# Performance work log

Measured on AMD Instinct MI355X. Metric: run time of the kernel, lower is better.

Reference implementation:

```python
import jax, jax.numpy as jnp
import numpy as np


def conv2d(x, w, pad):
    # x: [N,C,H,W], w: [O,I,kh,kw]
    return jax.lax.conv_general_dilated(
        x, w, window_strides=(1, 1), padding=[(pad, pad), (pad, pad)],
        dimension_numbers=("NCHW", "OIHW", "NCHW"))


def group_norm1(x, g, b, eps=1e-5):
    # GroupNorm(1, C): normalize over (C,H,W) per sample, per-channel affine
    mu = jnp.mean(x, axis=(1, 2, 3), keepdims=True)
    var = jnp.mean((x - mu) ** 2, axis=(1, 2, 3), keepdims=True)
    xn = (x - mu) * jax.lax.rsqrt(var + eps)
    return xn * g[None, :, None, None] + b[None, :, None, None]


def maxpool_3x3_s2(x):
    return jax.lax.reduce_window(
        x, -jnp.inf, jax.lax.max, (1, 1, 3, 3), (1, 1, 2, 2),
        ((0, 0), (0, 0), (1, 1), (1, 1)))


def hr2o_layer(x, wq, wk, wv, wo, g, b):
    # x: [N,C,H,W]; pairwise attention over the N ROIs at each (h,w)
    q = conv2d(x, wq, 1)
    k = conv2d(x, wk, 1)
    v = conv2d(x, wv, 1)
    scale = 1.0 / jnp.sqrt(jnp.asarray(x.shape[1], x.dtype))
    # torch: (q.unsqueeze(1) * k.unsqueeze(0)).sum(2) == einsum over channels
    att = jnp.einsum("nchw,mchw->nmhw", q, k) * scale  # [N,N,H,W]
    att = jax.nn.softmax(att, axis=1)                    # softmax over keys (dim=1)
    virt = jnp.einsum("nmhw,mchw->nchw", att, v)        # [N,C,H,W]
    virt = jax.nn.relu(group_norm1(virt, g, b))
    virt = conv2d(virt, wo, 1)
    return x + virt  # dropout is identity in eval mode


def setup_inputs() -> dict:
    key = jax.random.key(0)
    ks = jax.random.split(key, 12)
    N, C_R, H, W, HID, NCLS, DEPTH = 64, 1024, 16, 16, 512, 60, 2
    s = 0.02
    return {
        "bg_feats": jax.random.normal(ks[0], (C_R, H, W), jnp.float32),
        "actor_feats": jax.random.normal(ks[1], (N, C_R), jnp.float32),
        "w_conv1": jax.random.normal(ks[2], (HID, 2 * C_R, 1, 1), jnp.float32) * s,
        "w_conv2": jax.random.normal(ks[3], (HID, HID, 3, 3), jnp.float32) * s,
        "w_q": jax.random.normal(ks[4], (DEPTH, HID, HID, 3, 3), jnp.float32) * s,
        "w_k": jax.random.normal(ks[5], (DEPTH, HID, HID, 3, 3), jnp.float32) * s,
        "w_v": jax.random.normal(ks[6], (DEPTH, HID, HID, 3, 3), jnp.float32) * s,
        "w_o": jax.random.normal(ks[7], (DEPTH, HID, HID, 3, 3), jnp.float32) * s,
        "gamma": jnp.ones((DEPTH, HID), jnp.float32),
        "beta": jnp.zeros((DEPTH, HID), jnp.float32),
        "w_fc1": jax.random.normal(ks[8], (HID, C_R), jnp.float32) * s,
        "w_fc2": jax.random.normal(ks[9], (NCLS, 2 * HID), jnp.float32) * s,
    }


def reference(bg_feats, actor_feats, w_conv1, w_conv2, w_q, w_k, w_v, w_o,
              gamma, beta, w_fc1, w_fc2):
    N = actor_feats.shape[0]
    C_R, H, W = bg_feats.shape
    # bg repeated per ROI, actor features tiled over spatial dims
    bg = jnp.broadcast_to(bg_feats[None], (N, C_R, H, W))
    tiled = jnp.broadcast_to(actor_feats[:, :, None, None], (N, C_R, H, W))
    x = jnp.concatenate([bg, tiled], axis=1)           # [N, 2*C_R, H, W]
    x = jax.nn.relu(conv2d(x, w_conv1, 0))             # 1x1 -> [N,HID,H,W]
    x = jax.nn.relu(conv2d(x, w_conv2, 0))             # 3x3 pad=0 -> H-2,W-2
    x = maxpool_3x3_s2(x)                              # -> 7x7
    for d in range(w_q.shape[0]):
        x = hr2o_layer(x, w_q[d], w_k[d], w_v[d], w_o[d], gamma[d], beta[d])
    high_order = jnp.mean(x, axis=(2, 3))              # gap -> [N,HID]
    roi = jax.nn.relu(actor_feats @ w_fc1.T)           # [N,HID]
    out = jnp.concatenate([roi, high_order], axis=1) @ w_fc2.T  # [N,num_classes]
    return out
```

## Files before the change

### kernel.cpp

```cpp
#include <hip/hip_runtime.h>
#include <math.h>


typedef __bf16 bf16x8 __attribute__((ext_vector_type(8)));
typedef float  f32x4  __attribute__((ext_vector_type(4)));

#define NROI 64
#define CR   1024
#define HIDC 512
#define NCLS 60
#define PLANE (NROI * HIDC * 49)
#define ROWH 40
#define OCALL 4608
#define TAPSTR ((size_t)OCALL * 512)
#define WL (HIDC * HIDC * 9)
#define GNCNT 25088.0f

#if defined(__has_builtin)
#  if __has_builtin(__builtin_amdgcn_global_load_lds)
#    define HAVE_GLL 1
#  endif
#endif

__device__ __forceinline__ void stage16(const void* g, void* lds_base, int lane) {
#ifdef HAVE_GLL
    __builtin_amdgcn_global_load_lds(
        (const __attribute__((address_space(1))) unsigned int*)g,
        (__attribute__((address_space(3))) unsigned int*)lds_base, 16, 0, 0);
#else
    *(uint4*)((char*)lds_base + lane * 16) = *(const uint4*)g;
#endif
}

__device__ __forceinline__ float bf2f(unsigned short h) {
    union { unsigned u; float f; } x; x.u = (unsigned)h << 16; return x.f;
}

__global__ __launch_bounds__(256) void k_misc(
    const float* __restrict__ w2, const float* __restrict__ wq,
    const float* __restrict__ wk, const float* __restrict__ wv,
    const float* __restrict__ wo, const float* __restrict__ bg,
    __bf16* __restrict__ wAll, __bf16* __restrict__ inT7,
    __bf16* __restrict__ bgT)
{
    const int b = blockIdx.x, tid = threadIdx.x;
    if (b < 4608) {
        const int bid = b;
        const float* src;
        if (bid < 512) src = w2 + (size_t)bid * 4608;
        else if (bid < 2048) {
            const int r = bid - 512;
            const float* bb = r < 512 ? wq : (r < 1024 ? wk : wv);
            src = bb + (size_t)(r & 511) * 4608;
        } else if (bid < 2560) src = wo + (size_t)(bid - 2048) * 4608;
        else if (bid < 4096) {
            const int r = bid - 2560;
            const float* bb = r < 512 ? wq : (r < 1024 ? wk : wv);
            src = bb + WL + (size_t)(r & 511) * 4608;
        } else src = wo + WL + (size_t)(bid - 4096) * 4608;
        __shared__ float s[4608];
        const float4* s4 = (const float4*)src;
        for (int i = tid; i < 1152; i += 256) ((float4*)s)[i] = s4[i];
        __syncthreads();
        unsigned* dst = (unsigned*)wAll;
        const int c = tid * 2;
        const int swz = ((c >> 3) & 3) ^ ((bid >> 1) & 3);
        const size_t cidx = (size_t)(c >> 5) * 32 + swz * 8 + (c & 7);
#pragma unroll
        for (int t = 0; t < 9; ++t) {
            const unsigned short u0 = __builtin_bit_cast(unsigned short, (__bf16)s[c * 9 + t]);
            const unsigned short u1 = __builtin_bit_cast(unsigned short, (__bf16)s[(c + 1) * 9 + t]);
            dst[((size_t)t * TAPSTR + (size_t)bid * 512 + cidx) / 2] =
                ((unsigned)u1 << 16) | u0;
        }
    } else if (b < 5120) {
        const int k = b - 4608;
        const int n = k >> 3;
        const int j0 = (k & 7) * 4;
#pragma unroll
        for (int i = 0; i < 4; ++i) {
            const int jj = j0 + i;
            int sp;
            if (jj < 9) sp = jj;
            else if (jj < 18) sp = 63 + jj;
            else { const int t = jj - 18; sp = (1 + (t >> 1)) * 9 + (t & 1) * 8; }
            unsigned* d = (unsigned*)(inT7 + ((size_t)n * 81 + sp) * 512);
            d[tid] = 0u;
        }
    } else {
        const int cb = (b - 5120) * 8;
        const int p = tid;
        bf16x8 v;
#pragma unroll
        for (int j = 0; j < 8; ++j)
            v[j] = (__bf16)bg[(size_t)(cb + j) * 256 + p];
        *(bf16x8*)(bgT + (size_t)p * 1024 + cb) = v;
    }
}

__global__ __launch_bounds__(256, 2) void k_ab(
    const __bf16* __restrict__ bgT, const float* __restrict__ actor,
    const float* __restrict__ w1, const float* __restrict__ wfc1,
    float* __restrict__ A_T, float* __restrict__ Bp, float* __restrict__ roi)
{
    const int bx = blockIdx.x, by = blockIdx.y;
    const bool isA = bx < 4;
    const bool isRoi = (bx == 5);
    const int ocWg = by * 64;
    const int tid = threadIdx.x;
    const int w = tid >> 6, lane = tid & 63;
    const int q = lane >> 4, l16 = lane & 15;

    __shared__ __align__(16) __bf16 s_a[64 * ROWH];
    __shared__ __align__(16) __bf16 s_b[64 * ROWH];

    f32x4 acc[4];
#pragma unroll
    for (int nt = 0; nt < 4; ++nt) acc[nt] = (f32x4){0.f, 0.f, 0.f, 0.f};

    const int row = tid >> 2, part = tid & 3;
    for (int ch = 0; ch < 32; ++ch) {
        const int c0 = ch * 32;
        __syncthreads();
        if (isA) {
            const uint4 vv = *(const uint4*)(
                bgT + (size_t)(bx * 64 + row) * 1024 + c0 + part * 8);
            *(uint4*)(&s_a[row * ROWH + part * 8]) = vv;
        } else {
            const float* src = actor + (size_t)row * CR + c0 + part * 8;
            bf16x8 val;
#pragma unroll
            for (int j = 0; j < 8; ++j) val[j] = (__bf16)src[j];
            *(bf16x8*)(&s_a[row * ROWH + part * 8]) = val;
        }
        {
            const float* srcb = isRoi
                ? (wfc1 + (size_t)(ocWg + row) * CR + c0 + part * 8)
                : (w1 + (size_t)(ocWg + row) * (2 * CR)
                      + (isA ? 0 : CR) + c0 + part * 8);
            bf16x8 vb;
#pragma unroll
            for (int j = 0; j < 8; ++j) vb[j] = (__bf16)srcb[j];
            *(bf16x8*)(&s_b[row * ROWH + part * 8]) = vb;
        }
        __syncthreads();
        const bf16x8 af = *(const bf16x8*)(&s_a[(w * 16 + l16) * ROWH + q * 8]);
#pragma unroll
        for (int nt = 0; nt < 4; ++nt) {
            const bf16x8 bw = *(const bf16x8*)(&s_b[(nt * 16 + l16) * ROWH + q * 8]);
            acc[nt] = __builtin_amdgcn_mfma_f32_16x16x32_bf16(af, bw, acc[nt], 0, 0, 0);
        }
    }
#pragma unroll
    for (int r = 0; r < 4; ++r) {
#pragma unroll
        for (int nt = 0; nt < 4; ++nt) {
            const int mrow = w * 16 + q * 4 + r;
            const int oc = ocWg + nt * 16 + l16;
            if (isA)       A_T[(size_t)(bx * 64 + mrow) * 512 + oc] = acc[nt][r];
            else if (isRoi) roi[(size_t)mrow * 512 + oc] = fmaxf(acc[nt][r], 0.f);
            else           Bp[(size_t)mrow * 512 + oc] = acc[nt][r];
        }
    }
}

__global__ __launch_bounds__(256) void k_prep_in2(
    const float* __restrict__ A_T, const float* __restrict__ B,
    __bf16* __restrict__ dst)
{
    const int vn = blockIdx.x;
    const int n = vn >> 2, quad = vn & 3;
    const int sp0 = blockIdx.y * 27;
    const float b0 = B[n * HIDC + threadIdx.x];
    const float b1 = B[n * HIDC + 256 + threadIdx.x];
    for (int sp = sp0; sp < sp0 + 27; ++sp) {
        const int r = sp / 9, w = sp % 9;
        const int p16 = ((quad >> 1) * 7 + r) * 16 + (quad & 1) * 7 + w;
        __bf16* d = dst + ((size_t)vn * 81 + sp) * 512;
        d[threadIdx.x]       = (__bf16)fmaxf(A_T[p16 * HIDC + threadIdx.x] + b0, 0.f);
        d[256 + threadIdx.x] = (__bf16)fmaxf(A_T[p16 * HIDC + 256 + threadIdx.x] + b1, 0.f);
    }
}

template<int VN, bool GNIN>
__global__ __launch_bounds__(256, 2) void k_conv_mfma(
    const __bf16* __restrict__ inT,
    const float* __restrict__ vin,
    const float* __restrict__ statsRaw,
    const float* __restrict__ gamma, const float* __restrict__ beta,
    const __bf16* __restrict__ wAll, int ocBaseGl,
    const float* __restrict__ resid, float* __restrict__ outf,
    __bf16* __restrict__ outb, __bf16* __restrict__ inT7out,
    float* __restrict__ zeroStats, float* __restrict__ gapOut,
    float* __restrict__ gapZero, int mode)
{
    constexpr int MT = (VN == 4) ? 4 : ((VN == 2) ? 2 : 1);
    const int tid = threadIdx.x;
    const int w = tid >> 6, lane = tid & 63;
    const int q = lane >> 4, l16 = lane & 15;
    const int vn_l = (VN == 4) ? w : ((VN == 2) ? (w & 1) : 0);
    const int mh   = (VN == 4) ? 0 : ((VN == 2) ? (w >> 1) : w);
    const int vnBase = blockIdx.x * VN;
    const int ocWg = blockIdx.y * 64;

    if (zeroStats && blockIdx.x == 0 && blockIdx.y == 0 && tid < 128)
        zeroStats[tid] = 0.f;
    if (gapZero && blockIdx.y == 0 && blockIdx.x < 16) {
        const float4 z = {0.f, 0.f, 0.f, 0.f};
        ((float4*)gapZero)[blockIdx.x * 512 + tid * 2]     = z;
        ((float4*)gapZero)[blockIdx.x * 512 + tid * 2 + 1] = z;
    }

    __shared__ __align__(16) __bf16 s_w[9 * 64 * 32];
    __shared__ __align__(16) __bf16 s_in[VN * 81 * ROWH];
    __shared__ float s_mi[VN][2];
    __shared__ float s_gb[GNIN ? 1024 : 4];

    if (GNIN) {
        for (int k = tid; k < 512; k += 256) {
            s_gb[k]       = gamma[k];
            s_gb[512 + k] = beta[k];
        }
        if (tid < VN) {
            const float S = statsRaw[(vnBase + tid) * 2];
            const float Q = statsRaw[(vnBase + tid) * 2 + 1];
            const float mean = S / GNCNT;
            const float var  = Q / GNCNT - mean * mean;
            s_mi[tid][0] = mean;
            s_mi[tid][1] = rsqrtf(var + 1e-5f);
        }
    }

    const int bSwz = (q ^ ((l16 >> 1) & 3)) << 3;
    int aBase[MT];
#pragma unroll
    for (int mt = 0; mt < MT; ++mt) {
        int p = (mh * MT + mt) * 16 + l16;
        p = p > 48 ? 48 : p;
        aBase[mt] = (vn_l * 81 + (p / 7) * 9 + (p % 7)) * ROWH + q * 8;
    }

    f32x4 acc[MT][4];
#pragma unroll
    for (int a = 0; a < MT; ++a)
#pragma unroll
        for (int b = 0; b < 4; ++b) acc[a][b] = (f32x4){0.f, 0.f, 0.f, 0.f};

    for (int ch = 0; ch < 16; ++ch) {
        const int c0 = ch * 32;
        __syncthreads();
#pragma unroll
        for (int i = 0; i < 9; ++i) {
            const int s0 = (w * 9 + i) * 64;
            const int s = s0 + lane;
            const int t = s >> 8;
            const int rem = s & 255;
            const int row = rem >> 2, part = rem & 3;
            const __bf16* g = wAll + (size_t)t * TAPSTR
                + (size_t)(ocBaseGl + ocWg + row) * 512 + c0 + part * 8;
            stage16(g, (char*)s_w + (size_t)s0 * 16, lane);
        }
        for (int idx = tid; idx < VN * 324; idx += 256) {
            const int vnl = idx / 324, rem = idx - vnl * 324;
            const int r = rem >> 2, part = rem & 3;
            if (GNIN) {
                const int rr = r / 9, cc = r % 9;
                bf16x8 val;
                if (rr >= 1 && rr <= 7 && cc >= 1 && cc <= 7) {
                    const int p = (rr - 1) * 7 + (cc - 1);
                    const float* src = vin +
                        ((size_t)(vnBase + vnl) * 49 + p) * 512 + c0 + part * 8;
                    const float m = s_mi[vnl][0], iv = s_mi[vnl][1];
#pragma unroll
                    for (int j = 0; j < 8; ++j)
                        val[j] = (__bf16)fmaxf(
                            (src[j] - m) * iv * s_gb[c0 + part * 8 + j]
                            + s_gb[512 + c0 + part * 8 + j], 0.f);
                } else {
#pragma unroll
                    for (int j = 0; j < 8; ++j) val[j] = (__bf16)0.f;
                }
                *(bf16x8*)(&s_in[(vnl * 81 + r) * ROWH + part * 8]) = val;
            } else {
                const uint4 vv = *(const uint4*)(
                    inT + ((size_t)(vnBase + vnl) * 81 + r) * 512 + c0 + part * 8);
                *(uint4*)(&s_in[(vnl * 81 + r) * ROWH + part * 8]) = vv;
            }
        }
        __syncthreads();
#pragma unroll
        for (int t = 0; t < 9; ++t) {
            const int tOffA = ((t / 3) * 9 + (t % 3)) * ROWH;
            bf16x8 bw[4];
#pragma unroll
            for (int nt = 0; nt < 4; ++nt)
                bw[nt] = *(const bf16x8*)(&s_w[(t * 64 + nt * 16 + l16) * 32 + bSwz]);
            bf16x8 af[MT];
#pragma unroll
            for (int mt = 0; mt < MT; ++mt)
                af[mt] = *(const bf16x8*)(&s_in[aBase[mt] + tOffA]);
#pragma unroll
            for (int mt = 0; mt < MT; ++mt)
#pragma unroll
                for (int nt = 0; nt < 4; ++nt)
                    acc[mt][nt] = __builtin_amdgcn_mfma_f32_16x16x32_bf16(
                        af[mt], bw[nt], acc[mt][nt], 0, 0, 0);
        }
    }

    const int vn = vnBase + vn_l;
    float gsum[4] = {0.f, 0.f, 0.f, 0.f};
#pragma unroll
    for (int mt = 0; mt < MT; ++mt) {
#pragma unroll
        for (int r = 0; r < 4; ++r) {
            const int p = (mh * MT + mt) * 16 + q * 4 + r;
            if (p >= 49) continue;
#pragma unroll
            for (int nt = 0; nt < 4; ++nt) {
                const int oc = ocWg + nt * 16 + l16;
                const float v = acc[mt][nt][r];
                if (mode == 2) {
                    const int n = vn >> 2, quad = vn & 3;
                    const int p14 = ((quad >> 1) * 7 + p / 7) * 14 + (quad & 1) * 7 + p % 7;
                    outb[((size_t)n * 196 + p14) * 512 + oc] = (__bf16)fmaxf(v, 0.f);
                } else if (mode == 1) {
                    const size_t addr = ((size_t)vn * 49 + p) * 512 + oc;
                    const float res = v + resid[addr];
                    if (!gapOut) outf[addr] = res;
                    gsum[nt] += res;
                    if (inT7out) {
                        const int sp = (p / 7 + 1) * 9 + (p % 7 + 1);
                        inT7out[((size_t)vn * 81 + sp) * 512 + oc] = (__bf16)res;
                    }
                } else {
                    const int conv = oc >> 9;
                    outb[(size_t)conv * PLANE + ((size_t)p * 64 + vn) * 512 + (oc & 511)]
                        = (__bf16)v;
                }
            }
        }
    }
    if (gapOut) {
#pragma unroll
        for (int nt = 0; nt < 4; ++nt)
            atomicAdd(gapOut + (size_t)vn * 512 + ocWg + nt * 16 + l16, gsum[nt]);
    }
}

__global__ __launch_bounds__(256) void k_pool_prep(
    const __bf16* __restrict__ x2, __bf16* __restrict__ inT7,
    float* __restrict__ xA)
{
    const int b = blockIdx.x;
    const int n = b / 49, p = b % 49;
    const int i = p / 7, j = p % 7;
    const int sp = (i + 1) * 9 + (j + 1);
#pragma unroll
    for (int k = 0; k < 2; ++k) {
        const int c = threadIdx.x + k * 256;
        float mx = -1e30f;
#pragma unroll
        for (int di = -1; di <= 1; ++di) {
            const int rr = 2 * i + di;
            if (rr < 0 || rr >= 14) continue;
#pragma unroll
            for (int dj = -1; dj <= 1; ++dj) {
                const int cc = 2 * j + dj;
                if (cc < 0 || cc >= 14) continue;
                mx = fmaxf(mx, (float)x2[((size_t)n * 196 + rr * 14 + cc) * 512 + c]);
            }
        }
        inT7[((size_t)n * 81 + sp) * 512 + c] = (__bf16)mx;
        xA[((size_t)n * 49 + p) * 512 + c] = mx;
    }
}

__global__ __launch_bounds__(256) void k_attvirt(
    const __bf16* __restrict__ qT, const __bf16* __restrict__ kT,
    const __bf16* __restrict__ vT, float* __restrict__ virt,
    float* __restrict__ statsRaw)
{
    const int p = blockIdx.y;
    const int w = threadIdx.x >> 6, m = threadIdx.x & 63;
    const int n = blockIdx.x * 4 + w;
    __shared__ float s_q[4][HIDC];
    __shared__ float s_a[4][64];
    {
        const uint4 v = ((const uint4*)(qT + ((size_t)p * 64 + n) * HIDC))[m];
        const unsigned* u = (const unsigned*)&v;
#pragma unroll
        for (int j = 0; j < 4; ++j) {
            s_q[w][m * 8 + 2 * j]     = bf2f((unsigned short)(u[j] & 0xffff));
            s_q[w][m * 8 + 2 * j + 1] = bf2f((unsigned short)(u[j] >> 16));
        }
    }
    __syncthreads();
    const uint4* krow = (const uint4*)(kT + ((size_t)p * 64 + m) * HIDC);
    float acc0 = 0.f, acc1 = 0.f;
    for (int i = 0; i < 64; ++i) {
        const uint4 v = krow[i];
        const unsigned* u = (const unsigned*)&v;
#pragma unroll
        for (int j = 0; j < 2; ++j) {
            acc0 = fmaf(s_q[w][i * 8 + 2 * j],     bf2f((unsigned short)(u[j] & 0xffff)), acc0);
            acc0 = fmaf(s_q[w][i * 8 + 2 * j + 1], bf2f((unsigned short)(u[j] >> 16)),    acc0);
        }
#pragma unroll
        for (int j = 2; j < 4; ++j) {
            acc1 = fmaf(s_q[w][i * 8 + 2 * j],     bf2f((unsigned short)(u[j] & 0xffff)), acc1);
            acc1 = fmaf(s_q[w][i * 8 + 2 * j + 1], bf2f((unsigned short)(u[j] >> 16)),    acc1);
        }
    }
    float acc = (acc0 + acc1) * 0.044194173824159216f;
    float mx = acc;
#pragma unroll
    for (int off = 32; off; off >>= 1) mx = fmaxf(mx, __shfl_xor(mx, off));
    const float e = expf(acc - mx);
    float s = e;
#pragma unroll
    for (int off = 32; off; off >>= 1) s += __shfl_xor(s, off);
    s_a[w][m] = e / s;
    __syncthreads();
    const int c0 = m * 8;
    float av[8];
#pragma unroll
    for (int j = 0; j < 8; ++j) av[j] = 0.f;
    for (int mm = 0; mm < 64; ++mm) {
        const float a = s_a[w][mm];
        const uint4 v = *(const uint4*)(vT + ((size_t)p * 64 + mm) * HIDC + c0);
        const unsigned* u = (const unsigned*)&v;
#pragma unroll
        for (int j = 0; j < 4; ++j) {
            av[2 * j]     = fmaf(a, bf2f((unsigned short)(u[j] & 0xffff)), av[2 * j]);
            av[2 * j + 1] = fmaf(a, bf2f((unsigned short)(u[j] >> 16)),    av[2 * j + 1]);
        }
    }
    float* o = virt + ((size_t)n * 49 + p) * 512 + c0;
    float ps = 0.f, pq = 0.f;
#pragma unroll
    for (int j = 0; j < 8; ++j) {
        o[j] = av[j];
        ps += av[j];
        pq = fmaf(av[j], av[j], pq);
    }
#pragma unroll
    for (int off = 32; off; off >>= 1) {
        ps += __shfl_xor(ps, off);
        pq += __shfl_xor(pq, off);
    }
    if (m == 0) {
        atomicAdd(statsRaw + n * 2, ps);
        atomicAdd(statsRaw + n * 2 + 1, pq);
    }
}

__global__ __launch_bounds__(256) void k_final(
    const float* __restrict__ roi, const float* __restrict__ gap,
    const float* __restrict__ wfc2, float* __restrict__ out)
{
    const int n = blockIdx.x, tid = threadIdx.x;
    __shared__ float s[1024];
    s[tid]       = roi[(size_t)n * 512 + tid];
    s[tid + 256] = roi[(size_t)n * 512 + 256 + tid];
    s[tid + 512] = gap[(size_t)n * 512 + tid] * (1.f / 49.f);
    s[tid + 768] = gap[(size_t)n * 512 + 256 + tid] * (1.f / 49.f);
    __syncthreads();
    if (tid < 240) {
        const int k = tid >> 2, part = tid & 3;
        const float4* w4 = (const float4*)(wfc2 + (size_t)k * 1024 + part * 256);
        const float4* s4 = (const float4*)(s + part * 256);
        float a0 = 0.f, a1 = 0.f, a2 = 0.f, a3 = 0.f;
        for (int i = 0; i < 64; ++i) {
            const float4 wv = w4[i], sv = s4[i];
            a0 = fmaf(wv.x, sv.x, a0); a1 = fmaf(wv.y, sv.y, a1);
            a2 = fmaf(wv.z, sv.z, a2); a3 = fmaf(wv.w, sv.w, a3);
        }
        float acc = (a0 + a1) + (a2 + a3);
        acc += __shfl_xor(acc, 1);
        acc += __shfl_xor(acc, 2);
        if (part == 0) out[n * NCLS + k] = acc;
    }
}

extern "C" void kernel_launch(void* const* d_in, const int* in_sizes, int n_in,
                              void* d_out, int out_size, void* d_ws, size_t ws_size,
                              hipStream_t stream) {
    const float* bg    = (const float*)d_in[0];
    const float* actor = (const float*)d_in[1];
    const float* w1    = (const float*)d_in[2];
    const float* w2    = (const float*)d_in[3];
    const float* wq    = (const float*)d_in[4];
    const float* wk    = (const float*)d_in[5];
    const float* wv    = (const float*)d_in[6];
    const float* wo    = (const float*)d_in[7];
    const float* gamma = (const float*)d_in[8];
    const float* beta  = (const float*)d_in[9];
    const float* wfc1  = (const float*)d_in[10];
    const float* wfc2  = (const float*)d_in[11];
    float* out = (float*)d_out;
    float* ws  = (float*)d_ws;

    float* A_T   = ws;
    float* Bp    = A_T + 131072;
    float* xA    = Bp + 32768;
    float* xB    = xA + PLANE;
    float* stats = xB + PLANE;
    float* roi   = stats + 128;
    float* gap   = roi + 32768;
    float* fend  = gap + 32768;
    __bf16* x2h  = (__bf16*)fend;
    float*  virt = (float*)x2h;
    __bf16* inT2 = x2h + 6422528;
    __bf16* qkvT = inT2;
    __bf16* inT7 = inT2 + 10616832;
    __bf16* wAll = inT7 + 2654208;
    __bf16* bgT  = wAll + (size_t)9 * OCALL * 512;

    k_misc<<<5248, 256, 0, stream>>>(w2, wq, wk, wv, wo, bg, wAll, inT7, bgT);
    k_ab<<<dim3(6, 8), 256, 0, stream>>>(bgT, actor, w1, wfc1, A_T, Bp, roi);
    k_prep_in2<<<dim3(256, 3), 256, 0, stream>>>(A_T, Bp, inT2);
    k_conv_mfma<4, false><<<dim3(64, 8), 256, 0, stream>>>(
        inT2, nullptr, nullptr, nullptr, nullptr, wAll, 0,
        nullptr, nullptr, x2h, nullptr, nullptr, nullptr, nullptr, 2);
    k_pool_prep<<<64 * 49, 256, 0, stream>>>(x2h, inT7, xA);

    float* xin = xA;
    float* xout = xB;
    for (int d = 0; d < 2; ++d) {
        k_conv_mfma<2, false><<<dim3(32, 24), 256, 0, stream>>>(
            inT7, nullptr, nullptr, nullptr, nullptr, wAll, 512 + d * 2048,
            nullptr, nullptr, qkvT, nullptr, stats, nullptr,
            d == 1 ? gap : nullptr, 0);
        k_attvirt<<<dim3(16, 49), 256, 0, stream>>>(
            qkvT, qkvT + PLANE, qkvT + 2 * PLANE, virt, stats);
        k_conv_mfma<1, true><<<dim3(64, 8), 256, 0, stream>>>(
            nullptr, virt, stats, gamma + d * HIDC, beta + d * HIDC,
            wAll, 2048 + d * 2048, xin, xout, nullptr,
            d == 0 ? inT7 : nullptr, nullptr,
            d == 1 ? gap : nullptr, nullptr, 1);
        float* t = xin; xin = xout; xout = t;
    }
    k_final<<<64, 256, 0, stream>>>(roi, gap, wfc2, out);
}
```

Baseline: 621.2 us.

## Add double-buffered software-pipelined conv kernel for conv2 and QKV convs

Introduces k_conv_pipe, a 3x3 conv MFMA kernel that double-buffers both the weight tap slices and the 32-channel input chunks in LDS. It prefetches the next tap or chunk with async global-to-LDS loads while the current one is computed, and uses counted vmcnt waits instead of full drains. The goal is to hide global memory latency behind MFMA work in the conv2 and QKV convolutions. It also raises the occupancy hint to 3 for the VN=2 variant and uses XOR swizzled LDS layouts. The hand-tuned waitcnt counts are fragile: if they are wrong, reads can race with the loads.

```diff
diff --git a/kernel.cpp b/kernel.cpp
--- a/kernel.cpp
+++ b/kernel.cpp
@@ -182,6 +182,150 @@
     }
 }
 
+template<int VN, int MODE>
+__global__ __launch_bounds__(256, (VN == 4) ? 2 : 3) void k_conv_pipe(
+    const __bf16* __restrict__ inT,
+    const __bf16* __restrict__ wAll, int ocBaseGl,
+    __bf16* __restrict__ outb,
+    float* __restrict__ zeroStats, float* __restrict__ gapZero)
+{
+    constexpr int MT = (VN == 4) ? 4 : 2;
+    constexpr int SLOTS = VN * 324;
+    constexpr int NSUB = (SLOTS + 255) / 256;
+    constexpr int SBUF = NSUB * 256;
+    const int tid = threadIdx.x;
+    const int w = tid >> 6, lane = tid & 63;
+    const int q = lane >> 4, l16 = lane & 15;
+    const int vn_l = (VN == 4) ? w : (w & 1);
+    const int mh   = (VN == 4) ? 0 : (w >> 1);
+    const int vnBase = blockIdx.x * VN;
+    const int ocWg = blockIdx.y * 64;
+
+    if (zeroStats && blockIdx.x == 0 && blockIdx.y == 0 && tid < 128)
+        zeroStats[tid] = 0.f;
+    if (gapZero && blockIdx.y == 0 && blockIdx.x < 16) {
+        const float4 z = {0.f, 0.f, 0.f, 0.f};
+        ((float4*)gapZero)[blockIdx.x * 512 + tid * 2]     = z;
+        ((float4*)gapZero)[blockIdx.x * 512 + tid * 2 + 1] = z;
+    }
+
+    __shared__ __align__(16) __bf16 s_w[2 * 2048];
+    __shared__ __align__(16) __bf16 s_in[2 * SBUF * 8];
+
+    unsigned iGo[NSUB];
+#pragma unroll
+    for (int s = 0; s < NSUB; ++s) {
+        int idx = tid + s * 256;
+        if (idx > SLOTS - 1) idx = SLOTS - 1;
+        const int vnl = idx / 324, rem = idx - vnl * 324;
+        const int r = rem >> 2, part = rem & 3;
+        iGo[s] = (unsigned)(((vnBase + vnl) * 81 + r) * 512
+                            + ((part ^ (r & 3)) * 8));
+    }
+    const unsigned wGo = (unsigned)((ocBaseGl + ocWg + (tid >> 2)) * 512
+                                    + (tid & 3) * 8);
+    const int bOff = l16 * 32 + ((q ^ ((l16 >> 1) & 3)) << 3);
+
+    int aLoc[MT];
+#pragma unroll
+    for (int mt = 0; mt < MT; ++mt) {
+        int p = (mh * MT + mt) * 16 + l16;
+        p = p > 48 ? 48 : p;
+        aLoc[mt] = (p / 7) * 9 + (p % 7);
+    }
+    const int vb81 = vn_l * 81;
+
+    f32x4 acc[MT][4];
+#pragma unroll
+    for (int a = 0; a < MT; ++a)
+#pragma unroll
+        for (int b = 0; b < 4; ++b) acc[a][b] = (f32x4){0.f, 0.f, 0.f, 0.f};
+
+#pragma unroll
+    for (int s = 0; s < NSUB; ++s)
+        stage16(inT + iGo[s],
+                (char*)s_in + (size_t)(s * 256 + w * 64) * 16, lane);
+    stage16(wAll + wGo, (char*)s_w + (size_t)w * 1024, lane);
+
+    for (int ch = 0; ch < 16; ++ch) {
+        const int c0 = ch * 32;
+        const int chPar = ch & 1;
+        const int nxt = chPar ^ 1;
+#pragma unroll
+        for (int t = 0; t < 9; ++t) {
+            {
+                const int tapN = (t + 1) % 9;
+                const int cc = (t == 8) ? (c0 + 32) : c0;
+                const int parN = (chPar + t + 1) & 1;
+                stage16(wAll + (size_t)tapN * TAPSTR + wGo + cc,
+                        (char*)s_w + (size_t)parN * 4096 + (size_t)w * 1024,
+                        lane);
+            }
+            if (t < NSUB)
+                stage16(inT + iGo[t] + c0 + 32,
+                        (char*)s_in + (size_t)nxt * (SBUF * 16)
+                                    + (size_t)(t * 256 + w * 64) * 16, lane);
+            const int Wt = (VN == 4)
+                ? ((t == 0) ? 2 : (t <= 5) ? 3 : (t == 6) ? 2 : 1)
+                : ((t == 0) ? 2 : (t <= 2) ? 3 : (t == 3) ? 2 : 1);
+            if (Wt == 3)      asm volatile("s_waitcnt vmcnt(3)" ::: "memory");
+            else if (Wt == 2) asm volatile("s_waitcnt vmcnt(2)" ::: "memory");
+            else              asm volatile("s_waitcnt vmcnt(1)" ::: "memory");
+            __builtin_amdgcn_sched_barrier(0);
+            __builtin_amdgcn_s_barrier();
+            __builtin_amdgcn_sched_barrier(0);
+            {
+                const int par = (chPar + t) & 1;
+                const int DT = (t / 3) * 9 + (t % 3);
+                bf16x8 bw[4];
+#pragma unroll
+                for (int nt = 0; nt < 4; ++nt)
+                    bw[nt] = *(const bf16x8*)(&s_w[par * 2048 + nt * 512 + bOff]);
+                bf16x8 af[MT];
+#pragma unroll
+                for (int mt = 0; mt < MT; ++mt) {
+                    const int rl = aLoc[mt] + DT;
+                    const int col = (q ^ (rl & 3)) << 3;
+                    af[mt] = *(const bf16x8*)(
+                        &s_in[chPar * (SBUF * 8) + (vb81 + rl) * 32 + col]);
+                }
+#pragma unroll
+                for (int mt = 0; mt < MT; ++mt)
+#pragma unroll
+                    for (int nt = 0; nt < 4; ++nt)
+                        acc[mt][nt] = __builtin_amdgcn_mfma_f32_16x16x32_bf16(
+                            af[mt], bw[nt], acc[mt][nt], 0, 0, 0);
+            }
+            __builtin_amdgcn_sched_barrier(0);
+            __builtin_amdgcn_s_barrier();
+        }
+    }
+
+    const int vn = vnBase + vn_l;
+#pragma unroll
+    for (int mt = 0; mt < MT; ++mt) {
+#pragma unroll
+        for (int r = 0; r < 4; ++r) {
+            const int p = (mh * MT + mt) * 16 + q * 4 + r;
+            if (p >= 49) continue;
+#pragma unroll
+            for (int nt = 0; nt < 4; ++nt) {
+                const int oc = ocWg + nt * 16 + l16;
+                const float v = acc[mt][nt][r];
+                if (MODE == 2) {
+                    const int n = vn >> 2, quad = vn & 3;
+                    const int p14 = ((quad >> 1) * 7 + p / 7) * 14 + (quad & 1) * 7 + p % 7;
+                    outb[((size_t)n * 196 + p14) * 512 + oc] = (__bf16)fmaxf(v, 0.f);
+                } else {
+                    const int conv = oc >> 9;
+                    outb[(size_t)conv * PLANE + ((size_t)p * 64 + vn) * 512 + (oc & 511)]
+                        = (__bf16)v;
+                }
+            }
+        }
+    }
+}
+
 template<int VN, bool GNIN>
 __global__ __launch_bounds__(256, 2) void k_conv_mfma(
     const __bf16* __restrict__ inT,
@@ -520,18 +664,16 @@
     k_misc<<<5248, 256, 0, stream>>>(w2, wq, wk, wv, wo, bg, wAll, inT7, bgT);
     k_ab<<<dim3(6, 8), 256, 0, stream>>>(bgT, actor, w1, wfc1, A_T, Bp, roi);
     k_prep_in2<<<dim3(256, 3), 256, 0, stream>>>(A_T, Bp, inT2);
-    k_conv_mfma<4, false><<<dim3(64, 8), 256, 0, stream>>>(
-        inT2, nullptr, nullptr, nullptr, nullptr, wAll, 0,
-        nullptr, nullptr, x2h, nullptr, nullptr, nullptr, nullptr, 2);
+    k_conv_pipe<4, 2><<<dim3(64, 8), 256, 0, stream>>>(
+        inT2, wAll, 0, x2h, nullptr, nullptr);
     k_pool_prep<<<64 * 49, 256, 0, stream>>>(x2h, inT7, xA);
 
     float* xin = xA;
     float* xout = xB;
     for (int d = 0; d < 2; ++d) {
-        k_conv_mfma<2, false><<<dim3(32, 24), 256, 0, stream>>>(
-            inT7, nullptr, nullptr, nullptr, nullptr, wAll, 512 + d * 2048,
-            nullptr, nullptr, qkvT, nullptr, stats, nullptr,
-            d == 1 ? gap : nullptr, 0);
+        k_conv_pipe<2, 0><<<dim3(32, 24), 256, 0, stream>>>(
+            inT7, wAll, 512 + d * 2048, qkvT, stats,
+            d == 1 ? gap : nullptr);
         k_attvirt<<<dim3(16, 49), 256, 0, stream>>>(
             qkvT, qkvT + PLANE, qkvT + 2 * PLANE, virt, stats);
         k_conv_mfma<1, true><<<dim3(64, 8), 256, 0, stream>>>(
```

New measurement: 645.1 us. 1.04x slower.
